# Optimization experiments

Hardware: AMD Instinct MI355X
Metric: run time of the kernel (lower is better)

The kernel has to match this reference:

```python
import jax, jax.numpy as jnp
import numpy as np

TT_IN = (8, 8, 8, 8)
TT_OUT = (8, 8, 8, 8)
TT_RANKS = (1, 32, 32, 32, 1)
BATCH = 4096
N_IN = int(np.prod(TT_IN))     # 4096
N_OUT = int(np.prod(TT_OUT))   # 4096
KERNEL_LEN = int(sum(TT_RANKS[k] * TT_IN[k] * TT_OUT[k] * TT_RANKS[k + 1]
                     for k in range(len(TT_IN))))  # 135168


def setup_inputs() -> dict:
    key = jax.random.key(0)
    kx, kk = jax.random.split(key)
    x = jax.random.normal(kx, (BATCH, N_IN), dtype=jnp.float32)
    # flat packed TT cores (the layer stores all cores in one 1-D weight)
    kernel = 0.02 * jax.random.normal(kk, (KERNEL_LEN,), dtype=jnp.float32)
    bias = jnp.zeros((N_OUT,), dtype=jnp.float32)
    return {"x": x, "kernel": kernel, "bias": bias}


def reference(x, kernel, bias):
    # Faithful translation of TensorTrainDense.call: iterate cores k = d-1 .. 0,
    # slicing the flat kernel from index 0 (matching the original code exactly).
    batch = x.shape[0]
    res = x
    idx = 0
    for k in range(len(TT_IN) - 1, -1, -1):
        m = TT_IN[k] * TT_RANKS[k + 1]   # contraction dim
        n = TT_RANKS[k] * TT_OUT[k]      # output dim of this core
        core = kernel[idx:idx + m * n].reshape(m, n)
        res = res.reshape(-1, m) @ core              # (-1, r_k*out_k)
        res = res.reshape(-1, TT_OUT[k]).T           # (out_k, -1)
        idx += m * n
    res = res.reshape(-1, batch).T                   # (batch, prod(out))
    return res + bias
```

## Files before the change

### kernel.cpp

```cpp
#include <hip/hip_runtime.h>
#include <hip/hip_bf16.h>

typedef unsigned short u16;
typedef __attribute__((ext_vector_type(8))) short  bf16x8;
typedef __attribute__((ext_vector_type(4))) float  fx4;

#define OFF_C0 0
#define OFF_C1 2048
#define OFF_C2 67584
#define OFF_C3 133120

static __device__ __forceinline__ u16 f2bf(float f) {
  union { __hip_bfloat16 h; u16 u; } cv;
  cv.h = __float2bfloat16(f);
  return cv.u;
}
static __device__ __forceinline__ float bf2f(u16 u) {
  union { u16 u; __hip_bfloat16 h; } cv;
  cv.u = u;
  return __bfloat162float(cv.h);
}

__global__ void build_w34T(const float* __restrict__ ker, float* __restrict__ w34T) {
  int t = blockIdx.x * 256 + threadIdx.x;
  int i34 = t & 63, c = t >> 6;
  int a2 = c >> 6, o3 = (c >> 3) & 7, o4 = c & 7;
  int i3 = i34 >> 3, i4 = i34 & 7;
  float s = 0.f;
#pragma unroll 8
  for (int a3 = 0; a3 < 32; ++a3) {
    float k1 = ker[OFF_C1 + (i3 * 32 + a3) * 256 + a2 * 8 + o3];
    float k0 = ker[OFF_C0 + i4 * 256 + a3 * 8 + o4];
    s += k1 * k0;
  }
  w34T[c * 64 + i34] = s;
}

__global__ void build_w234t2(const float* __restrict__ ker, const float* __restrict__ w34T,
                             u16* __restrict__ w234t) {
  int t = blockIdx.x * 256 + threadIdx.x;
  int i234 = t & 511, g = t >> 9;
  int a1 = g >> 3, o3 = g & 7;
  int i2 = i234 >> 6, i34 = i234 & 63;
  float acc[8][8];
#pragma unroll
  for (int a = 0; a < 8; ++a)
#pragma unroll
    for (int b = 0; b < 8; ++b) acc[a][b] = 0.f;
  for (int a2 = 0; a2 < 32; ++a2) {
    float w[8];
#pragma unroll
    for (int o4 = 0; o4 < 8; ++o4)
      w[o4] = w34T[(a2 * 64 + o3 * 8 + o4) * 64 + i34];
#pragma unroll
    for (int o2 = 0; o2 < 8; ++o2) {
      float c2 = ker[OFF_C2 + (i2 * 32 + a2) * 256 + a1 * 8 + o2];
#pragma unroll
      for (int o4 = 0; o4 < 8; ++o4) acc[o2][o4] += c2 * w[o4];
    }
  }
#pragma unroll
  for (int o2 = 0; o2 < 8; ++o2) {
    int cg = a1 * 64 + o2 * 8 + o3;
#pragma unroll
    for (int o4 = 0; o4 < 8; ++o4)
      w234t[(cg * 8 + o4) * 512 + i234] = f2bf(acc[o2][o4]);
  }
}

__global__ void build_wt2(const float* __restrict__ ker, const u16* __restrict__ w234t,
                          u16* __restrict__ wt) {
  int t = blockIdx.x * 256 + threadIdx.x;
  int i234 = t & 511, j234 = t >> 9;
  float acc[8][8];
#pragma unroll
  for (int a = 0; a < 8; ++a)
#pragma unroll
    for (int b = 0; b < 8; ++b) acc[a][b] = 0.f;
  for (int a1 = 0; a1 < 32; ++a1) {
    float w = bf2f(w234t[(a1 * 512 + j234) * 512 + i234]);
#pragma unroll
    for (int i1 = 0; i1 < 8; ++i1) {
      const float* c3 = ker + OFF_C3 + (i1 * 32 + a1) * 8;
#pragma unroll
      for (int o1 = 0; o1 < 8; ++o1) acc[i1][o1] += c3[o1] * w;
    }
  }
#pragma unroll
  for (int o1 = 0; o1 < 8; ++o1)
#pragma unroll
    for (int i1 = 0; i1 < 8; ++i1)
      wt[(size_t)(o1 * 512 + j234) * 4096 + i1 * 512 + i234] = f2bf(acc[i1][o1]);
}

__global__ void x_to_bf16(const float* __restrict__ x, u16* __restrict__ xb) {
  int t = blockIdx.x * 256 + threadIdx.x;
  const fx4* p = (const fx4*)(x + (size_t)t * 8);
  fx4 v0 = p[0], v1 = p[1];
  u16 tmp[8];
#pragma unroll
  for (int q = 0; q < 4; ++q) tmp[q] = f2bf(v0[q]);
#pragma unroll
  for (int q = 0; q < 4; ++q) tmp[4 + q] = f2bf(v1[q]);
  typedef __attribute__((ext_vector_type(8))) u16 u16x8;
  *(u16x8*)(xb + (size_t)t * 8) = *(const u16x8*)tmp;
}

__device__ __forceinline__ void gld16(const u16* g, u16* l) {
  __builtin_amdgcn_global_load_lds((const __attribute__((address_space(1))) void*)g,
                                   (__attribute__((address_space(3))) void*)l, 16, 0, 0);
}

__global__ __launch_bounds__(512, 2) void gemm_bt2(const u16* __restrict__ A, const u16* __restrict__ Bt,
                                                   const float* __restrict__ bias, float* __restrict__ C) {
  __shared__ __align__(16) u16 sh[65536];

  const int tid = threadIdx.x;
  const int lane = tid & 63;
  const int wave = tid >> 6;
  const int wm = wave >> 2, wn = wave & 3;
  const int fr = lane & 15, fg = lane >> 4;

  const int bid = blockIdx.x;
  const int wg = (bid & 7) * 32 + (bid >> 3);
  const int bm = (wg >> 4) * 256, bn = (wg & 15) * 256;

  const int srow = tid >> 2;
  const int sco = (((tid & 3) ^ ((tid >> 3) & 3)) * 8);
  const size_t agA0 = (size_t)(bm + srow) * 4096 + sco;
  const size_t agA1 = agA0 + (size_t)128 * 4096;
  const size_t agB0 = (size_t)(bn + srow) * 4096 + sco;
  const size_t agB1 = agB0 + (size_t)128 * 4096;
  const int ldsW = wave * 512;

  fx4 acc[8][4];
#pragma unroll
  for (int m = 0; m < 8; ++m)
#pragma unroll
    for (int n = 0; n < 4; ++n) acc[m][n] = (fx4){0.f, 0.f, 0.f, 0.f};

  for (int pt = 0; pt < 3; ++pt) {
    u16* Aq = sh + pt * 8192;
    u16* Bq = sh + 32768 + pt * 8192;
    gld16(A + agA0 + pt * 32, Aq + ldsW);
    gld16(A + agA1 + pt * 32, Aq + ldsW + 4096);
    gld16(Bt + agB0 + pt * 32, Bq + ldsW);
    gld16(Bt + agB1 + pt * 32, Bq + ldsW + 4096);
  }
  asm volatile("s_waitcnt vmcnt(8)" ::: "memory");
  __builtin_amdgcn_s_barrier();

  for (int t = 0; t < 128; ++t) {
    u16* Ap = sh + (t & 3) * 8192;
    u16* Bp = sh + 32768 + (t & 3) * 8192;
    u16* Aq = sh + ((t + 3) & 3) * 8192;
    u16* Bq = sh + 32768 + ((t + 3) & 3) * 8192;
    const size_t ko = (size_t)(((t + 3) & 127) * 32);

    bf16x8 av[4], bv[4];
#pragma unroll
    for (int m = 0; m < 4; ++m) {
      const int R = wm * 128 + m * 16 + fr;
      av[m] = *(const bf16x8*)(Ap + R * 32 + ((fg ^ ((R >> 1) & 3)) * 8));
    }
#pragma unroll
    for (int n = 0; n < 4; ++n) {
      const int R = wn * 64 + n * 16 + fr;
      bv[n] = *(const bf16x8*)(Bp + R * 32 + ((fg ^ ((R >> 1) & 3)) * 8));
    }
    gld16(A + agA0 + ko, Aq + ldsW);
    gld16(A + agA1 + ko, Aq + ldsW + 4096);
    __builtin_amdgcn_s_barrier();
    __builtin_amdgcn_s_setprio(1);
#pragma unroll
    for (int m = 0; m < 4; ++m)
#pragma unroll
      for (int n = 0; n < 4; ++n)
        acc[m][n] = __builtin_amdgcn_mfma_f32_16x16x32_bf16(av[m], bv[n], acc[m][n], 0, 0, 0);
    __builtin_amdgcn_s_setprio(0);
    __builtin_amdgcn_s_barrier();

    bf16x8 aw[4];
#pragma unroll
    for (int m = 0; m < 4; ++m) {
      const int R = wm * 128 + 64 + m * 16 + fr;
      aw[m] = *(const bf16x8*)(Ap + R * 32 + ((fg ^ ((R >> 1) & 3)) * 8));
    }
    gld16(Bt + agB0 + ko, Bq + ldsW);
    gld16(Bt + agB1 + ko, Bq + ldsW + 4096);
    __builtin_amdgcn_s_barrier();
    __builtin_amdgcn_s_setprio(1);
#pragma unroll
    for (int m = 0; m < 4; ++m)
#pragma unroll
      for (int n = 0; n < 4; ++n)
        acc[4 + m][n] = __builtin_amdgcn_mfma_f32_16x16x32_bf16(aw[m], bv[n], acc[4 + m][n], 0, 0, 0);
    __builtin_amdgcn_s_setprio(0);
    asm volatile("s_waitcnt vmcnt(8)" ::: "memory");
    __builtin_amdgcn_s_barrier();
  }

  const int crow0 = bm + wm * 128 + fg * 4;
  const int ccol0 = bn + wn * 64 + fr;
#pragma unroll
  for (int n = 0; n < 4; ++n) {
    const int col = ccol0 + n * 16;
    const float bvl = bias[col];
#pragma unroll
    for (int mf = 0; mf < 8; ++mf) {
      const int r0 = crow0 + mf * 16;
#pragma unroll
      for (int q = 0; q < 4; ++q)
        C[(size_t)(r0 + q) * 4096 + col] = acc[mf][n][q] + bvl;
    }
  }
}

extern "C" void kernel_launch(void* const* d_in, const int* in_sizes, int n_in,
                              void* d_out, int out_size, void* d_ws, size_t ws_size,
                              hipStream_t stream) {
  const float* x    = (const float*)d_in[0];
  const float* ker  = (const float*)d_in[1];
  const float* bias = (const float*)d_in[2];
  float* out = (float*)d_out;

  char* ws = (char*)d_ws;
  u16*  xb    = (u16*)ws;
  u16*  wt    = (u16*)(ws + 33554432);
  u16*  w234t = (u16*)(ws + 67108864);
  float* w34T = (float*)(ws + 83886080);

  x_to_bf16   <<<8192, 256, 0, stream>>>(x, xb);
  build_w34T  <<<512, 256, 0, stream>>>(ker, w34T);
  build_w234t2<<<512, 256, 0, stream>>>(ker, w34T, w234t);
  build_wt2   <<<1024, 256, 0, stream>>>(ker, w234t, wt);
  gemm_bt2    <<<256, 512, 0, stream>>>(xb, wt, bias, out);
}
```

Baseline: 180.4 us.

## Restructure GEMM main loop into double-buffered 64-wide K steps and merge prep kernels

```diff
diff --git a/kernel.cpp b/kernel.cpp
--- a/kernel.cpp
+++ b/kernel.cpp
@@ -21,19 +21,33 @@
   return __bfloat162float(cv.h);
 }
 
-__global__ void build_w34T(const float* __restrict__ ker, float* __restrict__ w34T) {
-  int t = blockIdx.x * 256 + threadIdx.x;
-  int i34 = t & 63, c = t >> 6;
-  int a2 = c >> 6, o3 = (c >> 3) & 7, o4 = c & 7;
-  int i3 = i34 >> 3, i4 = i34 & 7;
-  float s = 0.f;
+__global__ void x_and_w34T(const float* __restrict__ x, u16* __restrict__ xb,
+                           const float* __restrict__ ker, float* __restrict__ w34T) {
+  if (blockIdx.x < 8192) {
+    int t = blockIdx.x * 256 + threadIdx.x;
+    const fx4* p = (const fx4*)(x + (size_t)t * 8);
+    fx4 v0 = p[0], v1 = p[1];
+    u16 tmp[8];
+#pragma unroll
+    for (int q = 0; q < 4; ++q) tmp[q] = f2bf(v0[q]);
+#pragma unroll
+    for (int q = 0; q < 4; ++q) tmp[4 + q] = f2bf(v1[q]);
+    typedef __attribute__((ext_vector_type(8))) u16 u16x8;
+    *(u16x8*)(xb + (size_t)t * 8) = *(const u16x8*)tmp;
+  } else {
+    int t = (blockIdx.x - 8192) * 256 + threadIdx.x;
+    int i34 = t & 63, c = t >> 6;
+    int a2 = c >> 6, o3 = (c >> 3) & 7, o4 = c & 7;
+    int i3 = i34 >> 3, i4 = i34 & 7;
+    float s = 0.f;
 #pragma unroll 8
-  for (int a3 = 0; a3 < 32; ++a3) {
-    float k1 = ker[OFF_C1 + (i3 * 32 + a3) * 256 + a2 * 8 + o3];
-    float k0 = ker[OFF_C0 + i4 * 256 + a3 * 8 + o4];
-    s += k1 * k0;
-  }
-  w34T[c * 64 + i34] = s;
+    for (int a3 = 0; a3 < 32; ++a3) {
+      float k1 = ker[OFF_C1 + (i3 * 32 + a3) * 256 + a2 * 8 + o3];
+      float k0 = ker[OFF_C0 + i4 * 256 + a3 * 8 + o4];
+      s += k1 * k0;
+    }
+    w34T[c * 64 + i34] = s;
+  }
 }
 
 __global__ void build_w234t2(const float* __restrict__ ker, const float* __restrict__ w34T,
@@ -93,25 +107,12 @@
       wt[(size_t)(o1 * 512 + j234) * 4096 + i1 * 512 + i234] = f2bf(acc[i1][o1]);
 }
 
-__global__ void x_to_bf16(const float* __restrict__ x, u16* __restrict__ xb) {
-  int t = blockIdx.x * 256 + threadIdx.x;
-  const fx4* p = (const fx4*)(x + (size_t)t * 8);
-  fx4 v0 = p[0], v1 = p[1];
-  u16 tmp[8];
-#pragma unroll
-  for (int q = 0; q < 4; ++q) tmp[q] = f2bf(v0[q]);
-#pragma unroll
-  for (int q = 0; q < 4; ++q) tmp[4 + q] = f2bf(v1[q]);
-  typedef __attribute__((ext_vector_type(8))) u16 u16x8;
-  *(u16x8*)(xb + (size_t)t * 8) = *(const u16x8*)tmp;
-}
-
 __device__ __forceinline__ void gld16(const u16* g, u16* l) {
   __builtin_amdgcn_global_load_lds((const __attribute__((address_space(1))) void*)g,
                                    (__attribute__((address_space(3))) void*)l, 16, 0, 0);
 }
 
-__global__ __launch_bounds__(512, 2) void gemm_bt2(const u16* __restrict__ A, const u16* __restrict__ Bt,
+__global__ __launch_bounds__(512, 2) void gemm_8ph(const u16* __restrict__ Ag, const u16* __restrict__ Bg,
                                                    const float* __restrict__ bias, float* __restrict__ C) {
   __shared__ __align__(16) u16 sh[65536];
 
@@ -133,44 +134,50 @@
   const size_t agB1 = agB0 + (size_t)128 * 4096;
   const int ldsW = wave * 512;
 
+#define ABASE(b, kh) (sh + ((b) * 2 + (kh)) * 8192)
+#define BBASE(b, kh) (sh + 32768 + ((b) * 2 + (kh)) * 8192)
+#define STAGE_A(b, kh, sp) do { const size_t c_ = (size_t)(((sp) & 63) * 64 + (kh) * 32); \
+    gld16(Ag + agA0 + c_, ABASE(b, kh) + ldsW); \
+    gld16(Ag + agA1 + c_, ABASE(b, kh) + ldsW + 4096); } while (0)
+#define STAGE_B(b, kh, sp) do { const size_t c_ = (size_t)(((sp) & 63) * 64 + (kh) * 32); \
+    gld16(Bg + agB0 + c_, BBASE(b, kh) + ldsW); \
+    gld16(Bg + agB1 + c_, BBASE(b, kh) + ldsW + 4096); } while (0)
+
+  int aoff[8], boff[4];
+#pragma unroll
+  for (int m = 0; m < 8; ++m) {
+    const int R = wm * 128 + m * 16 + fr;
+    aoff[m] = R * 32 + ((fg ^ ((R >> 1) & 3)) * 8);
+  }
+#pragma unroll
+  for (int n = 0; n < 4; ++n) {
+    const int R = wn * 64 + n * 16 + fr;
+    boff[n] = R * 32 + ((fg ^ ((R >> 1) & 3)) * 8);
+  }
+
   fx4 acc[8][4];
 #pragma unroll
   for (int m = 0; m < 8; ++m)
 #pragma unroll
     for (int n = 0; n < 4; ++n) acc[m][n] = (fx4){0.f, 0.f, 0.f, 0.f};
 
-  for (int pt = 0; pt < 3; ++pt) {
-    u16* Aq = sh + pt * 8192;
-    u16* Bq = sh + 32768 + pt * 8192;
-    gld16(A + agA0 + pt * 32, Aq + ldsW);
-    gld16(A + agA1 + pt * 32, Aq + ldsW + 4096);
-    gld16(Bt + agB0 + pt * 32, Bq + ldsW);
-    gld16(Bt + agB1 + pt * 32, Bq + ldsW + 4096);
-  }
-  asm volatile("s_waitcnt vmcnt(8)" ::: "memory");
+  STAGE_A(0, 0, 0);
+  STAGE_B(0, 0, 0);
+  STAGE_A(0, 1, 0);
+  STAGE_B(0, 1, 0);
+  asm volatile("s_waitcnt vmcnt(4)" ::: "memory");
   __builtin_amdgcn_s_barrier();
 
-  for (int t = 0; t < 128; ++t) {
-    u16* Ap = sh + (t & 3) * 8192;
-    u16* Bp = sh + 32768 + (t & 3) * 8192;
-    u16* Aq = sh + ((t + 3) & 3) * 8192;
-    u16* Bq = sh + 32768 + ((t + 3) & 3) * 8192;
-    const size_t ko = (size_t)(((t + 3) & 127) * 32);
-
+  auto kstep = [&](const int b, const int s) {
+    const int nb = 1 - b;
     bf16x8 av[4], bv[4];
 #pragma unroll
-    for (int m = 0; m < 4; ++m) {
-      const int R = wm * 128 + m * 16 + fr;
-      av[m] = *(const bf16x8*)(Ap + R * 32 + ((fg ^ ((R >> 1) & 3)) * 8));
-    }
-#pragma unroll
-    for (int n = 0; n < 4; ++n) {
-      const int R = wn * 64 + n * 16 + fr;
-      bv[n] = *(const bf16x8*)(Bp + R * 32 + ((fg ^ ((R >> 1) & 3)) * 8));
-    }
-    gld16(A + agA0 + ko, Aq + ldsW);
-    gld16(A + agA1 + ko, Aq + ldsW + 4096);
-    __builtin_amdgcn_s_barrier();
+    for (int m = 0; m < 4; ++m) av[m] = *(const bf16x8*)(ABASE(b, 0) + aoff[m]);
+#pragma unroll
+    for (int n = 0; n < 4; ++n) bv[n] = *(const bf16x8*)(BBASE(b, 0) + boff[n]);
+    STAGE_A(nb, 0, s + 1);
+    __builtin_amdgcn_s_barrier();
+    asm volatile("s_waitcnt lgkmcnt(0)" ::: "memory");
     __builtin_amdgcn_s_setprio(1);
 #pragma unroll
     for (int m = 0; m < 4; ++m)
@@ -179,25 +186,54 @@
         acc[m][n] = __builtin_amdgcn_mfma_f32_16x16x32_bf16(av[m], bv[n], acc[m][n], 0, 0, 0);
     __builtin_amdgcn_s_setprio(0);
     __builtin_amdgcn_s_barrier();
-
-    bf16x8 aw[4];
-#pragma unroll
-    for (int m = 0; m < 4; ++m) {
-      const int R = wm * 128 + 64 + m * 16 + fr;
-      aw[m] = *(const bf16x8*)(Ap + R * 32 + ((fg ^ ((R >> 1) & 3)) * 8));
-    }
-    gld16(Bt + agB0 + ko, Bq + ldsW);
-    gld16(Bt + agB1 + ko, Bq + ldsW + 4096);
-    __builtin_amdgcn_s_barrier();
-    __builtin_amdgcn_s_setprio(1);
-#pragma unroll
-    for (int m = 0; m < 4; ++m)
-#pragma unroll
-      for (int n = 0; n < 4; ++n)
-        acc[4 + m][n] = __builtin_amdgcn_mfma_f32_16x16x32_bf16(aw[m], bv[n], acc[4 + m][n], 0, 0, 0);
-    __builtin_amdgcn_s_setprio(0);
-    asm volatile("s_waitcnt vmcnt(8)" ::: "memory");
-    __builtin_amdgcn_s_barrier();
+#pragma unroll
+    for (int m = 0; m < 4; ++m) av[m] = *(const bf16x8*)(ABASE(b, 0) + aoff[4 + m]);
+    STAGE_B(nb, 0, s + 1);
+    __builtin_amdgcn_s_barrier();
+    asm volatile("s_waitcnt lgkmcnt(0)" ::: "memory");
+    __builtin_amdgcn_s_setprio(1);
+#pragma unroll
+    for (int m = 0; m < 4; ++m)
+#pragma unroll
+      for (int n = 0; n < 4; ++n)
+        acc[4 + m][n] = __builtin_amdgcn_mfma_f32_16x16x32_bf16(av[m], bv[n], acc[4 + m][n], 0, 0, 0);
+    __builtin_amdgcn_s_setprio(0);
+    asm volatile("s_waitcnt vmcnt(4)" ::: "memory");
+    __builtin_amdgcn_s_barrier();
+#pragma unroll
+    for (int m = 0; m < 4; ++m) av[m] = *(const bf16x8*)(ABASE(b, 1) + aoff[m]);
+#pragma unroll
+    for (int n = 0; n < 4; ++n) bv[n] = *(const bf16x8*)(BBASE(b, 1) + boff[n]);
+    STAGE_A(nb, 1, s + 1);
+    __builtin_amdgcn_s_barrier();
+    asm volatile("s_waitcnt lgkmcnt(0)" ::: "memory");
+    __builtin_amdgcn_s_setprio(1);
+#pragma unroll
+    for (int m = 0; m < 4; ++m)
+#pragma unroll
+      for (int n = 0; n < 4; ++n)
+        acc[m][n] = __builtin_amdgcn_mfma_f32_16x16x32_bf16(av[m], bv[n], acc[m][n], 0, 0, 0);
+    __builtin_amdgcn_s_setprio(0);
+    __builtin_amdgcn_s_barrier();
+#pragma unroll
+    for (int m = 0; m < 4; ++m) av[m] = *(const bf16x8*)(ABASE(b, 1) + aoff[4 + m]);
+    STAGE_B(nb, 1, s + 1);
+    __builtin_amdgcn_s_barrier();
+    asm volatile("s_waitcnt lgkmcnt(0)" ::: "memory");
+    __builtin_amdgcn_s_setprio(1);
+#pragma unroll
+    for (int m = 0; m < 4; ++m)
+#pragma unroll
+      for (int n = 0; n < 4; ++n)
+        acc[4 + m][n] = __builtin_amdgcn_mfma_f32_16x16x32_bf16(av[m], bv[n], acc[4 + m][n], 0, 0, 0);
+    __builtin_amdgcn_s_setprio(0);
+    asm volatile("s_waitcnt vmcnt(4)" ::: "memory");
+    __builtin_amdgcn_s_barrier();
+  };
+
+  for (int it = 0; it < 32; ++it) {
+    kstep(0, it * 2);
+    kstep(1, it * 2 + 1);
   }
 
   const int crow0 = bm + wm * 128 + fg * 4;
@@ -214,6 +250,10 @@
         C[(size_t)(r0 + q) * 4096 + col] = acc[mf][n][q] + bvl;
     }
   }
+#undef ABASE
+#undef BBASE
+#undef STAGE_A
+#undef STAGE_B
 }
 
 extern "C" void kernel_launch(void* const* d_in, const int* in_sizes, int n_in,
@@ -230,9 +270,8 @@
   u16*  w234t = (u16*)(ws + 67108864);
   float* w34T = (float*)(ws + 83886080);
 
-  x_to_bf16   <<<8192, 256, 0, stream>>>(x, xb);
-  build_w34T  <<<512, 256, 0, stream>>>(ker, w34T);
+  x_and_w34T  <<<8704, 256, 0, stream>>>(x, xb, ker, w34T);
   build_w234t2<<<512, 256, 0, stream>>>(ker, w34T, w234t);
   build_wt2   <<<1024, 256, 0, stream>>>(ker, w234t, wt);
-  gemm_bt2    <<<256, 512, 0, stream>>>(xb, wt, bias, out);
-}
+  gemm_8ph    <<<256, 512, 0, stream>>>(xb, wt, bias, out);
+}
```

Measured after the change: 181.3 us. About the same (+0.5%).
